# Kernel tuning notes

Hardware: AMD Instinct MI355X
Metric: run time of the kernel (lower is better)

The kernel has to match this reference:

```python
import jax, jax.numpy as jnp
import numpy as np

N = 1024        # total atoms
H = 256         # hidden_dim
L = 512         # latent_dim
NG = 50         # n_gaussians
NI = 3          # n_interactions
CUTOFF = 5.0
MAXZ = 100
B = 16          # molecules (N // 64 atoms each)

CENTERS = jnp.linspace(0.0, CUTOFF, NG)
WIDTH = 0.5 * (CUTOFF / NG)   # scalar, same for all gaussians
LN_EPS = 1e-5

def gelu(x):
    return jax.nn.gelu(x, approximate=False)  # torch default GELU is exact erf

def setup_inputs() -> dict:
    key = jax.random.key(0)
    ks = jax.random.split(key, 24)
    s = 0.05
    inp = {
        'z': jax.random.randint(ks[0], (N,), 0, MAXZ),
        'pos': jax.random.uniform(ks[1], (N, 3), dtype=jnp.float32) * 10.0,  # 10 A box
        'batch': jnp.arange(N, dtype=jnp.int32) // (N // B),
        'emb': jax.random.normal(ks[2], (MAXZ, H), dtype=jnp.float32),
        # per-interaction params stacked over layer axis (NI)
        'fw1': jax.random.normal(ks[3], (NI, NG, H), dtype=jnp.float32) * s,
        'fb1': jnp.zeros((NI, H), jnp.float32),
        'fw2': jax.random.normal(ks[4], (NI, H, H), dtype=jnp.float32) * s,
        'fb2': jnp.zeros((NI, H), jnp.float32),
        'aw1': jax.random.normal(ks[5], (NI, H, H), dtype=jnp.float32) * s,
        'ab1': jnp.zeros((NI, H), jnp.float32),
        'aw2': jax.random.normal(ks[6], (NI, H, H), dtype=jnp.float32) * s,
        'ab2': jnp.zeros((NI, H), jnp.float32),
        # projection head
        'pw1': jax.random.normal(ks[7], (H, H), dtype=jnp.float32) * s,
        'pb1': jnp.zeros((H,), jnp.float32),
        'pw2': jax.random.normal(ks[8], (H, L), dtype=jnp.float32) * s,
        'pb2': jnp.zeros((L,), jnp.float32),
        'ln_g': jnp.ones((L,), jnp.float32),
        'ln_b': jnp.zeros((L,), jnp.float32),
    }
    return inp

def _interaction(h, pos, fw1, fb1, fw2, fb2, aw1, ab1, aw2, ab2):
    diff = pos[None, :, :] - pos[:, None, :]              # [N,N,3]
    dist = jnp.linalg.norm(diff, axis=-1)                  # [N,N]
    mask = (dist < CUTOFF) & (dist > 1e-6)                 # [N,N]
    rbf = jnp.exp(-((dist[..., None] - CENTERS) ** 2) / (2.0 * WIDTH ** 2))  # [N,N,NG]
    W = gelu(rbf @ fw1 + fb1) @ fw2 + fb2                  # [N,N,H] filter MLP
    Wm = W * mask[..., None].astype(W.dtype)
    # agg[i,c] = sum_j Wm[i,j,c] * h[j,c]
    agg = jnp.einsum('ijc,jc->ic', Wm, h)
    return gelu(agg @ aw1 + ab1) @ aw2 + ab2

def reference(z, pos, batch, emb, fw1, fb1, fw2, fb2, aw1, ab1, aw2, ab2,
              pw1, pb1, pw2, pb2, ln_g, ln_b):
    h = emb[z]                                             # [N,H]
    for i in range(NI):
        h = h + _interaction(h, pos, fw1[i], fb1[i], fw2[i], fb2[i],
                             aw1[i], ab1[i], aw2[i], ab2[i])
    pooled = jax.ops.segment_sum(h, batch, num_segments=B)  # [B,H]
    x = gelu(pooled @ pw1 + pb1) @ pw2 + pb2               # [B,L]
    mu = jnp.mean(x, axis=-1, keepdims=True)
    var = jnp.var(x, axis=-1, keepdims=True)
    return (x - mu) / jnp.sqrt(var + LN_EPS) * ln_g + ln_b
```

## Files before the change

### kernel.cpp

```cpp
#include <hip/hip_runtime.h>
#include <hip/hip_fp16.h>
#include <math.h>

#define N 1024
#define H 256
#define L 512
#define NG 50
#define NI 3
#define B 16
#define NBINS 4096
#define CUT 5.0f
#define BPB 16
#define TROWS (NBINS + 1)
#define MATB 4
#define CAP 768
#define APAD 264

typedef __attribute__((ext_vector_type(8))) short bf16x8;
typedef __attribute__((ext_vector_type(4))) float f32x4;

#define FMA4(A_, S_, V_) do { \
    (A_).x = fmaf((S_), (V_).x, (A_).x); (A_).y = fmaf((S_), (V_).y, (A_).y); \
    (A_).z = fmaf((S_), (V_).z, (A_).z); (A_).w = fmaf((S_), (V_).w, (A_).w); } while (0)

__device__ __forceinline__ float gelu_f(float x) {
    return 0.5f * x * (1.0f + erff(x * 0.70710678118654752f));
}
__device__ __forceinline__ unsigned short f2bf(float f) {
    unsigned u = __float_as_uint(f);
    unsigned r = (u + 0x7fffu + ((u >> 16) & 1u)) >> 16;
    return (unsigned short)r;
}

__global__ void __launch_bounds__(256) nbrbuild_k(
        const int* __restrict__ z, const float* __restrict__ emb,
        const float* __restrict__ pos, float* __restrict__ h,
        __half* __restrict__ hhf, int* __restrict__ meta,
        int* __restrict__ cnts) {
    int i = blockIdx.x;
    int tid = threadIdx.x;
    float v = emb[z[i] * H + tid];
    h[i * H + tid] = v;
    hhf[i * H + tid] = __float2half(v);

    __shared__ int sCnt;
    __shared__ int sMeta[CAP];
    if (tid == 0) sCnt = 0;
    __syncthreads();
    float pix = pos[i * 3 + 0], piy = pos[i * 3 + 1], piz = pos[i * 3 + 2];
    const float invd = (float)NBINS / CUT;
    for (int r = 0; r < 4; ++r) {
        int j = tid + r * 256;
        float dx = pos[j * 3 + 0] - pix;
        float dy = pos[j * 3 + 1] - piy;
        float dz = pos[j * 3 + 2] - piz;
        float d = sqrtf(dx * dx + dy * dy + dz * dz);
        if (d < CUT && d > 1e-6f) {
            int bin = (int)(d * invd);
            if (bin > NBINS - 1) bin = NBINS - 1;
            int idx = atomicAdd(&sCnt, 1);
            sMeta[idx] = j | (bin << 10);
        }
    }
    __syncthreads();
    int cnt = sCnt;
    int pc = (cnt + 31) & ~31;
    for (int t = cnt + tid; t < pc; t += 256)
        sMeta[t] = i | (NBINS << 10);
    __syncthreads();
    for (int t = tid; t < pc; t += 256)
        meta[(size_t)i * CAP + t] = sMeta[t];
    if (tid == 0) cnts[i] = pc;
}

__global__ void bweights_k(const float* __restrict__ fw2,
                           unsigned short* __restrict__ Bt,
                           __half* __restrict__ Wtb) {
    int blk = blockIdx.x;
    int l = blk / H, ch = blk % H;
    int k = threadIdx.x;
    float v = fw2[((size_t)l * H + k) * H + ch];
    Bt[((size_t)l * H + ch) * H + k] = f2bf(v);
    if (k == 0)
        Wtb[((size_t)l * TROWS + NBINS) * H + ch] = __float2half(0.f);
}

__global__ void __launch_bounds__(256) table_k(
        const float* __restrict__ fw1, const float* __restrict__ fb1,
        const unsigned short* __restrict__ Bt, const float* __restrict__ fb2,
        __half* __restrict__ Wtb) {
    const int bpl = NBINS / BPB;
    int layer = blockIdx.x / bpl;
    int blk = blockIdx.x % bpl;
    int b0 = blk * BPB;
    int tid = threadIdx.x;
    int wid = tid >> 6, lane = tid & 63;
    int c4 = lane * 4;
    int ub = wid * 4;
    const float* lfw1 = fw1 + layer * NG * H;
    __half* lWt = Wtb + (size_t)layer * TROWS * H;

    __shared__ __align__(16) float sRbf[BPB][56];
    __shared__ __align__(16) unsigned short sAb[BPB][APAD];
    const float delta = CUT / (float)NBINS;
    for (int idx = tid; idx < BPB * NG; idx += 256) {
        int u = idx & 15;
        int k = idx >> 4;
        float d = ((float)(b0 + u) + 0.5f) * delta;
        float t = d - (float)k * (CUT / 49.0f);
        sRbf[u][k] = expf(t * t * -200.0f);
    }
    __syncthreads();

    float4 acc1[4];
    #pragma unroll
    for (int u = 0; u < 4; ++u) acc1[u] = make_float4(0.f, 0.f, 0.f, 0.f);
    for (int kq = 0; kq < 12; ++kq) {
        int k = kq * 4;
        float4 r0 = *(const float4*)&sRbf[ub + 0][k];
        float4 r1 = *(const float4*)&sRbf[ub + 1][k];
        float4 r2 = *(const float4*)&sRbf[ub + 2][k];
        float4 r3 = *(const float4*)&sRbf[ub + 3][k];
        float4 q0 = *(const float4*)(lfw1 + (k + 0) * H + c4);
        float4 q1 = *(const float4*)(lfw1 + (k + 1) * H + c4);
        float4 q2 = *(const float4*)(lfw1 + (k + 2) * H + c4);
        float4 q3 = *(const float4*)(lfw1 + (k + 3) * H + c4);
        FMA4(acc1[0], r0.x, q0); FMA4(acc1[0], r0.y, q1);
        FMA4(acc1[0], r0.z, q2); FMA4(acc1[0], r0.w, q3);
        FMA4(acc1[1], r1.x, q0); FMA4(acc1[1], r1.y, q1);
        FMA4(acc1[1], r1.z, q2); FMA4(acc1[1], r1.w, q3);
        FMA4(acc1[2], r2.x, q0); FMA4(acc1[2], r2.y, q1);
        FMA4(acc1[2], r2.z, q2); FMA4(acc1[2], r2.w, q3);
        FMA4(acc1[3], r3.x, q0); FMA4(acc1[3], r3.y, q1);
        FMA4(acc1[3], r3.z, q2); FMA4(acc1[3], r3.w, q3);
    }
    for (int k = 48; k < NG; ++k) {
        float4 q = *(const float4*)(lfw1 + k * H + c4);
        #pragma unroll
        for (int u = 0; u < 4; ++u) FMA4(acc1[u], sRbf[ub + u][k], q);
    }
    float4 b1 = *(const float4*)(fb1 + layer * H + c4);
    #pragma unroll
    for (int u = 0; u < 4; ++u) {
        ushort4 g;
        g.x = f2bf(gelu_f(acc1[u].x + b1.x));
        g.y = f2bf(gelu_f(acc1[u].y + b1.y));
        g.z = f2bf(gelu_f(acc1[u].z + b1.z));
        g.w = f2bf(gelu_f(acc1[u].w + b1.w));
        *(ushort4*)&sAb[ub + u][c4] = g;
    }
    __syncthreads();

    int m = lane & 15;
    int quad = lane >> 4;
    bf16x8 afr[8];
    #pragma unroll
    for (int c = 0; c < 8; ++c)
        afr[c] = *(const bf16x8*)&sAb[m][c * 32 + quad * 8];
    #pragma unroll
    for (int ct = 0; ct < 4; ++ct) {
        int chn = (wid * 4 + ct) * 16 + m;
        const bf16x8* Bv = (const bf16x8*)(Bt + ((size_t)layer * H + chn) * H);
        f32x4 acc = {0.f, 0.f, 0.f, 0.f};
        #pragma unroll
        for (int c = 0; c < 8; ++c)
            acc = __builtin_amdgcn_mfma_f32_16x16x32_bf16(afr[c], Bv[c * 4 + quad],
                                                          acc, 0, 0, 0);
        float bias = fb2[layer * H + chn];
        #pragma unroll
        for (int r = 0; r < 4; ++r) {
            int bin = b0 + quad * 4 + r;
            lWt[(size_t)bin * H + chn] = __float2half(acc[r] + bias);
        }
    }
}

__global__ void __launch_bounds__(256) pair_k(
    const __half* __restrict__ hhf, const __half* __restrict__ Wt,
    const int* __restrict__ gmeta, const int* __restrict__ cnts,
    float* __restrict__ aggP) {
    int tid = threadIdx.x;
    int wid = tid >> 6, lane = tid & 63;
    int c4 = lane * 4;
    int i = blockIdx.x >> 1;
    int half = blockIdx.x & 1;
    int stream = half * 4 + wid;

    __shared__ int sMeta[CAP];
    __shared__ __align__(16) float sPart[4][H];

    int pc = cnts[i];
    for (int t = tid; t < pc; t += 256)
        sMeta[t] = gmeta[(size_t)i * CAP + t];
    __syncthreads();

    float4 acc = make_float4(0.f, 0.f, 0.f, 0.f);
    int groups = pc >> 5;

    uint2 wA[4], wB[4];
    uint2 hA[4], hB[4];

    auto issue = [&](int g, uint2 (&wr)[4], uint2 (&hr)[4]) {
        #pragma unroll
        for (int s = 0; s < 4; ++s) {
            int n = stream + (g * 4 + s) * 8;
            int p = sMeta[n];
            int j = p & 1023;
            int bin = p >> 10;
            wr[s] = *(const uint2*)(Wt + (size_t)bin * H + c4);
            hr[s] = *(const uint2*)(hhf + (size_t)j * H + c4);
        }
    };
    auto consume = [&](uint2 (&wr)[4], uint2 (&hr)[4]) {
        #pragma unroll
        for (int s = 0; s < 4; ++s) {
            __half2 w01 = *(__half2*)&wr[s].x;
            __half2 w23 = *(__half2*)&wr[s].y;
            __half2 h01 = *(__half2*)&hr[s].x;
            __half2 h23 = *(__half2*)&hr[s].y;
            acc.x += __half2float(w01.x) * __half2float(h01.x);
            acc.y += __half2float(w01.y) * __half2float(h01.y);
            acc.z += __half2float(w23.x) * __half2float(h23.x);
            acc.w += __half2float(w23.y) * __half2float(h23.y);
        }
    };

    if (groups > 0) {
        issue(0, wA, hA);
        if (groups > 1) issue(1, wB, hB);
        for (int g = 0; g < groups; g += 2) {
            consume(wA, hA);
            if (g + 2 < groups) issue(g + 2, wA, hA);
            if (g + 1 < groups) {
                consume(wB, hB);
                if (g + 3 < groups) issue(g + 3, wB, hB);
            }
        }
    }
    *(float4*)&sPart[wid][c4] = acc;
    __syncthreads();
    aggP[((size_t)half * N + i) * H + tid] =
        sPart[0][tid] + sPart[1][tid] + sPart[2][tid] + sPart[3][tid];
}

__global__ void __launch_bounds__(512) mlp_k(
    const float* __restrict__ aggP, const float* __restrict__ hin,
    const float* __restrict__ aw1, const float* __restrict__ ab1,
    const float* __restrict__ aw2, const float* __restrict__ ab2,
    float* __restrict__ hout, __half* __restrict__ hhf_out) {
    int tid = threadIdx.x;
    int wid = tid >> 6, lane = tid & 63;
    int c4 = lane * 4;
    int i0 = blockIdx.x * MATB;
    __shared__ __align__(16) float sAT[H][MATB];
    __shared__ __align__(16) float sGT[H][MATB];
    __shared__ __align__(16) float sPart[8][MATB][H];

    if (tid < H) {
        #pragma unroll
        for (int r = 0; r < MATB; ++r)
            sAT[tid][r] = aggP[(size_t)(i0 + r) * H + tid]
                        + aggP[((size_t)N + i0 + r) * H + tid];
    }
    __syncthreads();

    int k0 = wid * 32;
    float4 acc[MATB];
    #pragma unroll
    for (int a = 0; a < MATB; ++a) acc[a] = make_float4(0.f, 0.f, 0.f, 0.f);
    #pragma unroll 8
    for (int k = 0; k < 32; ++k) {
        float4 q = *(const float4*)(aw1 + (k0 + k) * H + c4);
        float4 act = *(const float4*)&sAT[k0 + k][0];
        FMA4(acc[0], act.x, q); FMA4(acc[1], act.y, q);
        FMA4(acc[2], act.z, q); FMA4(acc[3], act.w, q);
    }
    #pragma unroll
    for (int a = 0; a < MATB; ++a)
        *(float4*)&sPart[wid][a][c4] = acc[a];
    __syncthreads();
    if (tid < H) {
        float b1 = ab1[tid];
        float g[MATB];
        #pragma unroll
        for (int a = 0; a < MATB; ++a) {
            float v = b1;
            #pragma unroll
            for (int s = 0; s < 8; ++s) v += sPart[s][a][tid];
            g[a] = gelu_f(v);
        }
        *(float4*)&sGT[tid][0] = make_float4(g[0], g[1], g[2], g[3]);
    }
    __syncthreads();
    #pragma unroll
    for (int a = 0; a < MATB; ++a) acc[a] = make_float4(0.f, 0.f, 0.f, 0.f);
    #pragma unroll 8
    for (int k = 0; k < 32; ++k) {
        float4 q = *(const float4*)(aw2 + (k0 + k) * H + c4);
        float4 act = *(const float4*)&sGT[k0 + k][0];
        FMA4(acc[0], act.x, q); FMA4(acc[1], act.y, q);
        FMA4(acc[2], act.z, q); FMA4(acc[3], act.w, q);
    }
    #pragma unroll
    for (int a = 0; a < MATB; ++a)
        *(float4*)&sPart[wid][a][c4] = acc[a];
    __syncthreads();
    if (tid < H) {
        float b2 = ab2[tid];
        #pragma unroll
        for (int a = 0; a < MATB; ++a) {
            float v = b2;
            #pragma unroll
            for (int s = 0; s < 8; ++s) v += sPart[s][a][tid];
            float hv = hin[(i0 + a) * H + tid] + v;
            hout[(i0 + a) * H + tid] = hv;
            hhf_out[(i0 + a) * H + tid] = __float2half(hv);
        }
    }
}

__global__ void __launch_bounds__(256) head_k(
        const float* __restrict__ h,
        const float* __restrict__ pw1, const float* __restrict__ pb1,
        const float* __restrict__ pw2, const float* __restrict__ pb2,
        const float* __restrict__ ln_g, const float* __restrict__ ln_b,
        float* __restrict__ out) {
    int b = blockIdx.x, tid = threadIdx.x;
    int wid = tid >> 6, lane = tid & 63;
    int c4 = lane * 4;
    __shared__ float sP[H];
    __shared__ __align__(16) float sPw[4][H];
    __shared__ float sG[H];
    __shared__ __align__(16) float sP2[4][L];
    __shared__ float sX[L];
    __shared__ float sRed[256];

    float4 p = make_float4(0.f, 0.f, 0.f, 0.f);
    #pragma unroll 4
    for (int a = 0; a < 16; ++a) {
        float4 hv = *(const float4*)(h + (b * 64 + wid * 16 + a) * H + c4);
        p.x += hv.x; p.y += hv.y; p.z += hv.z; p.w += hv.w;
    }
    *(float4*)&sPw[wid][c4] = p;
    __syncthreads();
    sP[tid] = sPw[0][tid] + sPw[1][tid] + sPw[2][tid] + sPw[3][tid];
    __syncthreads();

    int k0 = wid * 64;
    float4 acc = make_float4(0.f, 0.f, 0.f, 0.f);
    #pragma unroll 8
    for (int k = 0; k < 64; ++k) {
        float4 q = *(const float4*)(pw1 + (k0 + k) * H + c4);
        float s = sP[k0 + k];
        FMA4(acc, s, q);
    }
    *(float4*)&sPw[wid][c4] = acc;
    __syncthreads();
    sG[tid] = gelu_f(pb1[tid] + sPw[0][tid] + sPw[1][tid] + sPw[2][tid] + sPw[3][tid]);
    __syncthreads();

    float4 a0 = make_float4(0.f, 0.f, 0.f, 0.f);
    float4 a1 = make_float4(0.f, 0.f, 0.f, 0.f);
    #pragma unroll 4
    for (int k = 0; k < 64; ++k) {
        float s = sG[k0 + k];
        float4 q0 = *(const float4*)(pw2 + (k0 + k) * L + lane * 8);
        float4 q1 = *(const float4*)(pw2 + (k0 + k) * L + lane * 8 + 4);
        FMA4(a0, s, q0);
        FMA4(a1, s, q1);
    }
    *(float4*)&sP2[wid][lane * 8] = a0;
    *(float4*)&sP2[wid][lane * 8 + 4] = a1;
    __syncthreads();
    for (int r = 0; r < 2; ++r) {
        int l = tid + r * 256;
        sX[l] = pb2[l] + sP2[0][l] + sP2[1][l] + sP2[2][l] + sP2[3][l];
    }
    __syncthreads();

    sRed[tid] = sX[tid] + sX[tid + 256];
    __syncthreads();
    for (int off = 128; off > 0; off >>= 1) {
        if (tid < off) sRed[tid] += sRed[tid + off];
        __syncthreads();
    }
    float mu = sRed[0] / (float)L;
    __syncthreads();
    float d0 = sX[tid] - mu, d1 = sX[tid + 256] - mu;
    sRed[tid] = d0 * d0 + d1 * d1;
    __syncthreads();
    for (int off = 128; off > 0; off >>= 1) {
        if (tid < off) sRed[tid] += sRed[tid + off];
        __syncthreads();
    }
    float var = sRed[0] / (float)L;
    float rstd = rsqrtf(var + 1e-5f);
    for (int r = 0; r < 2; ++r) {
        int l = tid + r * 256;
        out[b * L + l] = (sX[l] - mu) * rstd * ln_g[l] + ln_b[l];
    }
}

extern "C" void kernel_launch(void* const* d_in, const int* in_sizes, int n_in,
                              void* d_out, int out_size, void* d_ws, size_t ws_size,
                              hipStream_t stream) {
    const int*   z    = (const int*)d_in[0];
    const float* pos  = (const float*)d_in[1];
    const float* emb  = (const float*)d_in[3];
    const float* fw1  = (const float*)d_in[4];
    const float* fb1  = (const float*)d_in[5];
    const float* fw2  = (const float*)d_in[6];
    const float* fb2  = (const float*)d_in[7];
    const float* aw1  = (const float*)d_in[8];
    const float* ab1  = (const float*)d_in[9];
    const float* aw2  = (const float*)d_in[10];
    const float* ab2  = (const float*)d_in[11];
    const float* pw1  = (const float*)d_in[12];
    const float* pb1  = (const float*)d_in[13];
    const float* pw2  = (const float*)d_in[14];
    const float* pb2  = (const float*)d_in[15];
    const float* ln_g = (const float*)d_in[16];
    const float* ln_b = (const float*)d_in[17];
    float* out = (float*)d_out;

    float* hA  = (float*)d_ws;
    float* hB  = hA + N * H;
    float* aggP = hB + N * H;
    __half* hhfA = (__half*)(aggP + 2 * N * H);
    __half* hhfB = hhfA + N * H;
    __half* Wtb  = hhfB + N * H;
    int* meta = (int*)(Wtb + (size_t)NI * TROWS * H);
    int* cnts = meta + (size_t)N * CAP;
    unsigned short* Bt = (unsigned short*)(cnts + N);

    nbrbuild_k<<<N, 256, 0, stream>>>(z, emb, pos, hA, hhfA, meta, cnts);
    bweights_k<<<NI * H, 256, 0, stream>>>(fw2, Bt, Wtb);
    table_k<<<NI * (NBINS / BPB), 256, 0, stream>>>(fw1, fb1, Bt, fb2, Wtb);
    float* hin = hA;  __half* hbin = hhfA;
    float* hout = hB; __half* hbout = hhfB;
    for (int it = 0; it < NI; ++it) {
        pair_k<<<2 * N, 256, 0, stream>>>(hbin, Wtb + (size_t)it * TROWS * H,
                                          meta, cnts, aggP);
        mlp_k<<<N / MATB, 512, 0, stream>>>(aggP, hin, aw1 + it * H * H, ab1 + it * H,
                                            aw2 + it * H * H, ab2 + it * H, hout, hbout);
        float* t1 = hin; hin = hout; hout = t1;
        __half* t2 = hbin; hbin = hbout; hbout = t2;
    }
    head_k<<<B, 256, 0, stream>>>(hin, pw1, pb1, pw2, pb2, ln_g, ln_b, out);
}
```

Baseline: 250.5 us.

## Halve filter table bins, merge setup kernels, stage fw1 in shared memory

Three changes at once. The distance-binned filter table is cut from 4096 to 2048 bins, halving the table-building work. The neighbour-build and fw2 transpose kernels are merged into one launch to save a launch. In the table kernel, the layer's fw1 weights are staged in shared memory instead of being read repeatedly from global memory. The coarser bins make the tabulated filter a rougher approximation of the exact per-distance filter, which may raise the numerical error.

```diff
diff --git a/kernel.cpp b/kernel.cpp
--- a/kernel.cpp
+++ b/kernel.cpp
@@ -8,7 +8,7 @@
 #define NG 50
 #define NI 3
 #define B 16
-#define NBINS 4096
+#define NBINS 2048
 #define CUT 5.0f
 #define BPB 16
 #define TROWS (NBINS + 1)
@@ -32,13 +32,23 @@
     return (unsigned short)r;
 }
 
-__global__ void __launch_bounds__(256) nbrbuild_k(
+__global__ void __launch_bounds__(256) setup_k(
         const int* __restrict__ z, const float* __restrict__ emb,
         const float* __restrict__ pos, float* __restrict__ h,
         __half* __restrict__ hhf, int* __restrict__ meta,
-        int* __restrict__ cnts) {
+        int* __restrict__ cnts, const float* __restrict__ fw2,
+        unsigned short* __restrict__ Bt, __half* __restrict__ Wtb) {
+    int tid = threadIdx.x;
+    if (blockIdx.x >= N) {
+        int blk = blockIdx.x - N;
+        int l = blk / H, ch = blk % H;
+        float v = fw2[((size_t)l * H + tid) * H + ch];
+        Bt[((size_t)l * H + ch) * H + tid] = f2bf(v);
+        if (tid == 0)
+            Wtb[((size_t)l * TROWS + NBINS) * H + ch] = __float2half(0.f);
+        return;
+    }
     int i = blockIdx.x;
-    int tid = threadIdx.x;
     float v = emb[z[i] * H + tid];
     h[i * H + tid] = v;
     hhf[i * H + tid] = __float2half(v);
@@ -71,18 +81,6 @@
     for (int t = tid; t < pc; t += 256)
         meta[(size_t)i * CAP + t] = sMeta[t];
     if (tid == 0) cnts[i] = pc;
-}
-
-__global__ void bweights_k(const float* __restrict__ fw2,
-                           unsigned short* __restrict__ Bt,
-                           __half* __restrict__ Wtb) {
-    int blk = blockIdx.x;
-    int l = blk / H, ch = blk % H;
-    int k = threadIdx.x;
-    float v = fw2[((size_t)l * H + k) * H + ch];
-    Bt[((size_t)l * H + ch) * H + k] = f2bf(v);
-    if (k == 0)
-        Wtb[((size_t)l * TROWS + NBINS) * H + ch] = __float2half(0.f);
 }
 
 __global__ void __launch_bounds__(256) table_k(
@@ -100,9 +98,15 @@
     const float* lfw1 = fw1 + layer * NG * H;
     __half* lWt = Wtb + (size_t)layer * TROWS * H;
 
+    __shared__ __align__(16) float sW1[NG][H];
     __shared__ __align__(16) float sRbf[BPB][56];
     __shared__ __align__(16) unsigned short sAb[BPB][APAD];
     const float delta = CUT / (float)NBINS;
+    for (int idx = tid; idx < NG * (H / 4); idx += 256) {
+        int k = idx >> 6;
+        int c = (idx & 63) * 4;
+        *(float4*)&sW1[k][c] = *(const float4*)(lfw1 + k * H + c);
+    }
     for (int idx = tid; idx < BPB * NG; idx += 256) {
         int u = idx & 15;
         int k = idx >> 4;
@@ -121,10 +125,10 @@
         float4 r1 = *(const float4*)&sRbf[ub + 1][k];
         float4 r2 = *(const float4*)&sRbf[ub + 2][k];
         float4 r3 = *(const float4*)&sRbf[ub + 3][k];
-        float4 q0 = *(const float4*)(lfw1 + (k + 0) * H + c4);
-        float4 q1 = *(const float4*)(lfw1 + (k + 1) * H + c4);
-        float4 q2 = *(const float4*)(lfw1 + (k + 2) * H + c4);
-        float4 q3 = *(const float4*)(lfw1 + (k + 3) * H + c4);
+        float4 q0 = *(const float4*)&sW1[k + 0][c4];
+        float4 q1 = *(const float4*)&sW1[k + 1][c4];
+        float4 q2 = *(const float4*)&sW1[k + 2][c4];
+        float4 q3 = *(const float4*)&sW1[k + 3][c4];
         FMA4(acc1[0], r0.x, q0); FMA4(acc1[0], r0.y, q1);
         FMA4(acc1[0], r0.z, q2); FMA4(acc1[0], r0.w, q3);
         FMA4(acc1[1], r1.x, q0); FMA4(acc1[1], r1.y, q1);
@@ -135,7 +139,7 @@
         FMA4(acc1[3], r3.z, q2); FMA4(acc1[3], r3.w, q3);
     }
     for (int k = 48; k < NG; ++k) {
-        float4 q = *(const float4*)(lfw1 + k * H + c4);
+        float4 q = *(const float4*)&sW1[k][c4];
         #pragma unroll
         for (int u = 0; u < 4; ++u) FMA4(acc1[u], sRbf[ub + u][k], q);
     }
@@ -433,8 +437,8 @@
     int* cnts = meta + (size_t)N * CAP;
     unsigned short* Bt = (unsigned short*)(cnts + N);
 
-    nbrbuild_k<<<N, 256, 0, stream>>>(z, emb, pos, hA, hhfA, meta, cnts);
-    bweights_k<<<NI * H, 256, 0, stream>>>(fw2, Bt, Wtb);
+    setup_k<<<N + NI * H, 256, 0, stream>>>(z, emb, pos, hA, hhfA, meta, cnts,
+                                            fw2, Bt, Wtb);
     table_k<<<NI * (NBINS / BPB), 256, 0, stream>>>(fw1, fb1, Bt, fb2, Wtb);
     float* hin = hA;  __half* hbin = hhfA;
     float* hout = hB; __half* hbout = hhfB;
```

New measurement: 236.8 us. -5.4%, faster.
